# Kernel optimization log

Measured on AMD Instinct MI355X. Metric: run time of the kernel, lower is better.

Reference implementation:

```python
import jax, jax.numpy as jnp
import numpy as np
from functools import partial

MAX_INSTANCES = 8


def _conv(x, W, b):
    y = jax.lax.conv_general_dilated(x, W, (1, 1), 'SAME',
                                     dimension_numbers=('NHWC', 'HWIO', 'NHWC'))
    return jax.nn.relu(y + b)


def _conv_stack(x, params):
    for W, b in params:
        x = _conv(x, W, b)
    return x


def _resize_and_pad(feat, info, bg_h, bg_w):
    # feat: (h, w, c); info: [y1, y2, x1, x2] fractions of bg size.
    # Bilinear resize (half-pixel centers, like tf.image.resize) of feat to
    # (y_size, x_size), then zero-pad into the (bg_h, bg_w) canvas at
    # (y_front, x_front). Expressed as a fixed-shape gather + validity mask
    # so it is jit-compatible despite data-dependent box sizes.
    h, w, _ = feat.shape
    y_size = jnp.maximum((bg_h * (info[1] - info[0])).astype(jnp.int32), 1)
    x_size = jnp.maximum((bg_w * (info[3] - info[2])).astype(jnp.int32), 1)
    y_front = (bg_h * info[0]).astype(jnp.int32)
    x_front = (bg_w * info[2]).astype(jnp.int32)

    def axis(bg_n, front, size, n_in):
        loc = jnp.arange(bg_n) - front
        valid = (loc >= 0) & (loc < size)
        src = (loc.astype(jnp.float32) + 0.5) * (n_in / size.astype(jnp.float32)) - 0.5
        src = jnp.clip(src, 0.0, n_in - 1.0)
        i0 = jnp.floor(src).astype(jnp.int32)
        i1 = jnp.minimum(i0 + 1, n_in - 1)
        return i0, i1, src - i0.astype(jnp.float32), valid

    y0, y1i, fy, vy = axis(bg_h, y_front, y_size, h)
    x0, x1i, fx, vx = axis(bg_w, x_front, x_size, w)
    g = lambda yi, xi: feat[yi][:, xi]  # (bg_h, bg_w, c)
    fy = fy[:, None, None]
    fx = fx[None, :, None]
    out = (g(y0, x0) * (1 - fy) * (1 - fx) + g(y0, x1i) * (1 - fy) * fx
           + g(y1i, x0) * fy * (1 - fx) + g(y1i, x1i) * fy * fx)
    return out * (vy[:, None] & vx[None, :]).astype(feat.dtype)[:, :, None]


def setup_inputs() -> dict:
    key = jax.random.key(0)
    ks = jax.random.split(key, 16)
    B, H, W, C = 4, 128, 128, 64
    h = w = 64
    hm = wm = 56
    U = 64
    MI = MAX_INSTANCES
    instance_feature = jax.random.normal(ks[0], (B, h, w, C, MI), jnp.float32)
    bg_feature = jax.random.normal(ks[1], (B, H, W, C), jnp.float32)
    # Valid boxes: 0 <= y1 < y2 <= 1, 0 <= x1 < x2 <= 1, layout (B, 4, MI).
    y1 = jax.random.uniform(ks[2], (B, 1, MI), minval=0.0, maxval=0.45)
    hh = jax.random.uniform(ks[3], (B, 1, MI), minval=0.2, maxval=0.5)
    x1 = jax.random.uniform(ks[4], (B, 1, MI), minval=0.0, maxval=0.45)
    ww = jax.random.uniform(ks[5], (B, 1, MI), minval=0.2, maxval=0.5)
    bbox = jnp.concatenate([y1, y1 + hh, x1, x1 + ww], axis=1)
    mrcnn_mask = jax.random.uniform(ks[6], (B, hm, wm, MI), jnp.float32)
    s = 0.05  # small weights keep exp() of relu conv outputs well-scaled
    return {
        'instance_feature': instance_feature,
        'bg_feature': bg_feature,
        'bbox': bbox,
        'mrcnn_mask': mrcnn_mask,
        'iW1': jax.random.normal(ks[7], (3, 3, C, U), jnp.float32) * s,
        'ib1': jnp.zeros((U,), jnp.float32),
        'iW2': jax.random.normal(ks[8], (3, 3, U, U), jnp.float32) * s,
        'ib2': jnp.zeros((U,), jnp.float32),
        'iW3': jax.random.normal(ks[9], (3, 3, U, 1), jnp.float32) * s,
        'ib3': jnp.zeros((1,), jnp.float32),
        'bW1': jax.random.normal(ks[10], (3, 3, C, U), jnp.float32) * s,
        'bb1': jnp.zeros((U,), jnp.float32),
        'bW2': jax.random.normal(ks[11], (3, 3, U, U), jnp.float32) * s,
        'bb2': jnp.zeros((U,), jnp.float32),
        'bW3': jax.random.normal(ks[12], (3, 3, U, 1), jnp.float32) * s,
        'bb3': jnp.zeros((1,), jnp.float32),
    }


def reference(instance_feature, bg_feature, bbox, mrcnn_mask,
              iW1, ib1, iW2, ib2, iW3, ib3,
              bW1, bb1, bW2, bb2, bW3, bb3):
    B, H, W, C = bg_feature.shape
    MI = instance_feature.shape[-1]
    h, w = instance_feature.shape[1], instance_feature.shape[2]
    # pack_instance -> conv stack -> unpack (kept as (B, MI, h, w, 1))
    packed = jnp.transpose(instance_feature, (0, 4, 1, 2, 3)).reshape(B * MI, h, w, C)
    iw = _conv_stack(packed, [(iW1, ib1), (iW2, ib2), (iW3, ib3)]).reshape(B, MI, h, w, 1)
    bgw = _conv_stack(bg_feature, [(bW1, bb1), (bW2, bb2), (bW3, bb3)])  # (B,H,W,1)

    rp = jax.vmap(jax.vmap(partial(_resize_and_pad, bg_h=H, bg_w=W)))
    bbox_t = jnp.transpose(bbox, (0, 2, 1))  # (B, MI, 4)
    rw = rp(iw, bbox_t)  # (B, MI, H, W, 1)
    full = jnp.broadcast_to(jnp.array([0.0, 1.0, 0.0, 1.0], jnp.float32), (B, MI, 4))
    rm = rp(jnp.moveaxis(mrcnn_mask, -1, 1)[..., None], full)  # (B, MI, H, W, 1)
    rsf = rp(jnp.moveaxis(instance_feature, -1, 1), bbox_t)  # (B, MI, H, W, C)

    ew = jnp.exp(rw) * rm          # per-instance exp weight, masked
    ew_bg = jnp.exp(bgw)           # (B, H, W, 1)
    denom = ew.sum(axis=1) + ew_bg  # (B, H, W, 1)
    return (ew_bg / denom) * bg_feature + jnp.sum(rsf * (ew / denom[:, None]), axis=1)
```

## Files before the change

### kernel.cpp

```cpp
#include <hip/hip_runtime.h>
#include <cstdint>

typedef short bf16x8 __attribute__((ext_vector_type(8)));
typedef float f32x4 __attribute__((ext_vector_type(4)));
typedef unsigned short u16;
typedef unsigned short u16x8 __attribute__((ext_vector_type(8)));
typedef unsigned int u32;

__device__ inline u16 f2bf(float f) {
  union { float f; unsigned u; } x; x.f = f;
  unsigned u = x.u + 0x7fffu + ((x.u >> 16) & 1u);
  return (u16)(u >> 16);
}
__device__ inline float bf2f(u16 h) {
  union { unsigned u; float f; } x; x.u = ((unsigned)h) << 16;
  return x.f;
}

__global__ __launch_bounds__(256) void prep_kernel(
    const float* __restrict__ inst, u16* __restrict__ pf,
    const float* __restrict__ w0, const float* __restrict__ w1,
    const float* __restrict__ w2, const float* __restrict__ w3,
    u16* __restrict__ wtr,
    const float* __restrict__ bgf, u16* __restrict__ bgp, int nT)
{
  if ((int)blockIdx.x < nT) {
    const int lane = threadIdx.x & 63;
    const int wvid = blockIdx.x * 4 + (threadIdx.x >> 6);
    const int b = wvid >> 12;
    const int pix = wvid & 4095;
    const float* s = inst + ((size_t)(b * 4096 + pix)) * 512 + lane * 8;
    float4 v0 = *(const float4*)s;
    float4 v1 = *(const float4*)(s + 4);
    float vals[8] = {v0.x, v0.y, v0.z, v0.w, v1.x, v1.y, v1.z, v1.w};
    #pragma unroll
    for (int i = 0; i < 8; i++)
      pf[(((size_t)(b * 8 + i)) * 4096 + pix) * 64 + lane] = f2bf(vals[i]);
  } else if ((int)blockIdx.x < nT + 576) {
    int id = (blockIdx.x - nT) * 256 + threadIdx.x;
    if (id >= 147456) return;
    int s = id / 36864;
    int r = id - s * 36864;
    int tap = r >> 12;
    int rc = r & 4095;
    int c = rc >> 6, u = rc & 63;
    const float* Ws = (s == 0) ? w0 : (s == 1) ? w1 : (s == 2) ? w2 : w3;
    wtr[(size_t)s * 36864 + ((size_t)tap * 64 + u) * 64 + c] =
        f2bf(Ws[((size_t)tap * 64 + c) * 64 + u]);
  } else {
    size_t id = (size_t)(blockIdx.x - nT - 576) * 256 + threadIdx.x;
    const float* s = bgf + id * 8;
    float4 v0 = *(const float4*)s;
    float4 v1 = *(const float4*)(s + 4);
    u16x8 o;
    o[0] = f2bf(v0.x); o[1] = f2bf(v0.y); o[2] = f2bf(v0.z); o[3] = f2bf(v0.w);
    o[4] = f2bf(v1.x); o[5] = f2bf(v1.y); o[6] = f2bf(v1.z); o[7] = f2bf(v1.w);
    *(u16x8*)(bgp + id * 8) = o;
  }
}

#define BOFF 41472
template<int SRC>
__device__ __forceinline__ void conv_body(
    char* smem, const void* __restrict__ inv, const u16* __restrict__ wtr,
    const float* __restrict__ bias, u16* __restrict__ out,
    int H, int W, int bid)
{
  const int tilesX = W >> 4;
  const int tilesPerImg = (H >> 4) * tilesX;
  const int img = bid / tilesPerImg;
  const int tile = bid - img * tilesPerImg;
  const int ty = (tile / tilesX) << 4;
  const int tx = (tile % tilesX) << 4;
  const int tid = threadIdx.x;

  for (int idx = tid; idx < 2592; idx += 256) {
    int hpix = idx >> 3;
    int c0 = (idx & 7) << 3;
    int hy = hpix / 18, hx = hpix - hy * 18;
    int gy = ty + hy - 1, gx = tx + hx - 1;
    u16x8 v = {0, 0, 0, 0, 0, 0, 0, 0};
    if (gy >= 0 && gy < H && gx >= 0 && gx < W) {
      if (SRC == 0) {
        const float* s = (const float*)inv + ((size_t)img * H * W + (size_t)gy * W + gx) * 64 + c0;
        #pragma unroll
        for (int j = 0; j < 8; j++) v[j] = f2bf(s[j]);
      } else if (SRC == 1) {
        const u16* s = (const u16*)inv + ((size_t)img * H * W + (size_t)gy * W + gx) * 64 + c0;
        v = *(const u16x8*)s;
      } else {
        int bb = img >> 3, ii = img & 7;
        const float* s = (const float*)inv + ((((size_t)bb * 64 + gy) * 64 + gx) * 64 + c0) * 8 + ii;
        #pragma unroll
        for (int j = 0; j < 8; j++) v[j] = f2bf(s[j * 8]);
      }
    }
    int byte = (hpix * 128 + c0 * 2) ^ ((hpix & 7) << 4);
    *(u16x8*)(smem + byte) = v;
  }

  const int lane = tid & 63;
  const int wv = tid >> 6;
  const int lrow = lane & 15;
  const int kg = lane >> 4;

  const int ch0 = tid, ch1 = tid + 256;
  const int bu0 = ch0 >> 3, bc0 = (ch0 & 7) << 3;
  const int bu1 = ch1 >> 3, bc1 = (ch1 & 7) << 3;
  const int bdst0 = BOFF + ((bu0 * 128 + bc0 * 2) ^ ((bu0 & 7) << 4));
  const int bdst1 = BOFF + ((bu1 * 128 + bc1 * 2) ^ ((bu1 & 7) << 4));

  {
    u16x8 n0 = *(const u16x8*)(wtr + (size_t)(0 * 64 + bu0) * 64 + bc0);
    u16x8 n1 = *(const u16x8*)(wtr + (size_t)(0 * 64 + bu1) * 64 + bc1);
    *(u16x8*)(smem + bdst0) = n0;
    *(u16x8*)(smem + bdst1) = n1;
  }
  __syncthreads();

  int pyv[4], pxv[4];
  #pragma unroll
  for (int mf = 0; mf < 4; mf++) {
    int p = wv * 64 + mf * 16 + lrow;
    pyv[mf] = p >> 4; pxv[mf] = p & 15;
  }

  f32x4 acc[4][4];
  #pragma unroll
  for (int a = 0; a < 4; a++)
    #pragma unroll
    for (int b = 0; b < 4; b++) { f32x4 z = {0.f, 0.f, 0.f, 0.f}; acc[a][b] = z; }

  for (int tap = 0; tap < 9; tap++) {
    u16x8 n0, n1;
    if (tap < 8) {
      n0 = *(const u16x8*)(wtr + (size_t)((tap + 1) * 64 + bu0) * 64 + bc0);
      n1 = *(const u16x8*)(wtr + (size_t)((tap + 1) * 64 + bu1) * 64 + bc1);
    }
    const int ky = tap / 3, kx = tap - ky * 3;
    #pragma unroll
    for (int ks = 0; ks < 2; ks++) {
      bf16x8 Bf[4];
      #pragma unroll
      for (int nf = 0; nf < 4; nf++) {
        int u = nf * 16 + lrow;
        int byte = BOFF + ((u * 128 + ks * 64 + kg * 16) ^ ((u & 7) << 4));
        Bf[nf] = *(const bf16x8*)(smem + byte);
      }
      #pragma unroll
      for (int mf = 0; mf < 4; mf++) {
        int hpix = (pyv[mf] + ky) * 18 + pxv[mf] + kx;
        int byte = (hpix * 128 + ks * 64 + kg * 16) ^ ((hpix & 7) << 4);
        bf16x8 Af = *(const bf16x8*)(smem + byte);
        #pragma unroll
        for (int nf = 0; nf < 4; nf++)
          acc[mf][nf] = __builtin_amdgcn_mfma_f32_16x16x32_bf16(Af, Bf[nf], acc[mf][nf], 0, 0, 0);
      }
    }
    __syncthreads();
    if (tap < 8) {
      *(u16x8*)(smem + bdst0) = n0;
      *(u16x8*)(smem + bdst1) = n1;
      __syncthreads();
    }
  }

  float bv[4];
  #pragma unroll
  for (int nf = 0; nf < 4; nf++) bv[nf] = bias[nf * 16 + lrow];

  const size_t obase = (size_t)img * H * W;
  #pragma unroll
  for (int mf = 0; mf < 4; mf++) {
    #pragma unroll
    for (int j = 0; j < 4; j++) {
      int p = wv * 64 + mf * 16 + kg * 4 + j;
      int oy = ty + (p >> 4), ox = tx + (p & 15);
      u16* op = out + (obase + (size_t)oy * W + ox) * 64 + lrow;
      #pragma unroll
      for (int nf = 0; nf < 4; nf++)
        op[nf * 16] = f2bf(fmaxf(acc[mf][nf][j] + bv[nf], 0.0f));
    }
  }
}

template<int S1, int S2>
__global__ __launch_bounds__(256) void conv_dual(
    const void* in1, const u16* w1, const float* b1, u16* o1, int H1, int W1, int split,
    const void* in2, const u16* w2, const float* b2, u16* o2, int H2, int W2)
{
  extern __shared__ float4 smem_f4[];
  char* smem = (char*)smem_f4;
  if ((int)blockIdx.x < split)
    conv_body<S1>(smem, in1, w1, b1, o1, H1, W1, blockIdx.x);
  else
    conv_body<S2>(smem, in2, w2, b2, o2, H2, W2, blockIdx.x - split);
}

__device__ __forceinline__ void conv3_body(
    char* smem, const u16* __restrict__ in, const float* __restrict__ W3,
    const float* __restrict__ b3, float* __restrict__ out, int H, int W, int bid)
{
  float* wlds = (float*)(smem + 41472);
  const int tilesX = W >> 4;
  const int tilesPerImg = (H >> 4) * tilesX;
  const int img = bid / tilesPerImg;
  const int tile = bid - img * tilesPerImg;
  const int ty = (tile / tilesX) << 4;
  const int tx = (tile % tilesX) << 4;
  const int tid = threadIdx.x;

  for (int idx = tid; idx < 2592; idx += 256) {
    int hpix = idx >> 3;
    int c0 = (idx & 7) << 3;
    int hy = hpix / 18, hx = hpix - hy * 18;
    int gy = ty + hy - 1, gx = tx + hx - 1;
    u16x8 v = {0, 0, 0, 0, 0, 0, 0, 0};
    if (gy >= 0 && gy < H && gx >= 0 && gx < W)
      v = *(const u16x8*)(in + ((size_t)img * H * W + (size_t)gy * W + gx) * 64 + c0);
    int byte = (hpix * 128 + c0 * 2) ^ ((hpix & 7) << 4);
    *(u16x8*)(smem + byte) = v;
  }
  for (int idx = tid; idx < 576; idx += 256) wlds[idx] = W3[idx];
  __syncthreads();

  const int py = tid >> 4, px = tid & 15;
  float acc = 0.0f;
  #pragma unroll
  for (int ky = 0; ky < 3; ky++) {
    #pragma unroll
    for (int kx = 0; kx < 3; kx++) {
      const int hpix = (py + ky) * 18 + (px + kx);
      const float* wp = wlds + (ky * 3 + kx) * 64;
      #pragma unroll
      for (int cg = 0; cg < 8; cg++) {
        int byte = (hpix * 128 + cg * 16) ^ ((hpix & 7) << 4);
        u16x8 v = *(const u16x8*)(smem + byte);
        #pragma unroll
        for (int j = 0; j < 8; j++)
          acc = fmaf(bf2f(v[j]), wp[cg * 8 + j], acc);
      }
    }
  }
  out[(size_t)img * H * W + (size_t)(ty + py) * W + (tx + px)] =
      fmaxf(acc + b3[0], 0.0f);
}

__global__ __launch_bounds__(256) void conv3_dual(
    const u16* in1, const float* W31, const float* b31, float* o1, int H1, int W1, int split,
    const u16* in2, const float* W32, const float* b32, float* o2, int H2, int W2)
{
  extern __shared__ float4 smem_f4[];
  char* smem = (char*)smem_f4;
  if ((int)blockIdx.x < split)
    conv3_body(smem, in1, W31, b31, o1, H1, W1, blockIdx.x);
  else
    conv3_body(smem, in2, W32, b32, o2, H2, W2, blockIdx.x - split);
}

__global__ __launch_bounds__(256) void precompute_params(
    const float* __restrict__ bbox, const float* __restrict__ mask,
    const float* __restrict__ iw, const float* __restrict__ bgw,
    float* __restrict__ pp_wbg, float* __restrict__ pp_wi,
    u32* __restrict__ pp_yx, float* __restrict__ pp_fy, float* __restrict__ pp_fx)
{
  const int gpix = blockIdx.x * 256 + threadIdx.x;
  const int b = gpix >> 14;
  const int p = gpix & 16383;
  const int Y = p >> 7, X = p & 127;

  float msy = ((float)Y + 0.5f) * 0.4375f - 0.5f;
  msy = fminf(fmaxf(msy, 0.0f), 55.0f);
  int my0 = (int)floorf(msy); int my1 = min(my0 + 1, 55); float fmy = msy - (float)my0;
  float msx = ((float)X + 0.5f) * 0.4375f - 0.5f;
  msx = fminf(fmaxf(msx, 0.0f), 55.0f);
  int mx0 = (int)floorf(msx); int mx1 = min(mx0 + 1, 55); float fmx = msx - (float)mx0;

  const float ewbg = expf(bgw[gpix]);
  float denom = ewbg;
  float wi_l[8];
  u32 yx_l[8];
  float fy_l[8], fx_l[8];

  #pragma unroll
  for (int i = 0; i < 8; i++) {
    float by1 = bbox[(b * 4 + 0) * 8 + i];
    float by2 = bbox[(b * 4 + 1) * 8 + i];
    float bx1 = bbox[(b * 4 + 2) * 8 + i];
    float bx2 = bbox[(b * 4 + 3) * 8 + i];
    int ysz = max((int)(128.0f * (by2 - by1)), 1);
    int xsz = max((int)(128.0f * (bx2 - bx1)), 1);
    int yfr = (int)(128.0f * by1);
    int xfr = (int)(128.0f * bx1);
    int ly = Y - yfr, lx = X - xfr;
    bool valid = (ly >= 0) && (ly < ysz) && (lx >= 0) && (lx < xsz);
    float rwv = 0.0f;
    int y0 = 0, y1i = 0, x0 = 0, x1i = 0;
    float fy = 0.0f, fx = 0.0f;
    if (valid) {
      float sy = ((float)ly + 0.5f) * (64.0f / (float)ysz) - 0.5f;
      sy = fminf(fmaxf(sy, 0.0f), 63.0f);
      y0 = (int)floorf(sy); y1i = min(y0 + 1, 63); fy = sy - (float)y0;
      float sx = ((float)lx + 0.5f) * (64.0f / (float)xsz) - 0.5f;
      sx = fminf(fmaxf(sx, 0.0f), 63.0f);
      x0 = (int)floorf(sx); x1i = min(x0 + 1, 63); fx = sx - (float)x0;
      const float* iwp = iw + ((size_t)(b * 8 + i)) * 4096;
      float v00 = iwp[y0 * 64 + x0],  v01 = iwp[y0 * 64 + x1i];
      float v10 = iwp[y1i * 64 + x0], v11 = iwp[y1i * 64 + x1i];
      rwv = v00 * (1.f - fy) * (1.f - fx) + v01 * (1.f - fy) * fx
          + v10 * fy * (1.f - fx)         + v11 * fy * fx;
    }
    const float* mp = mask + (size_t)b * 56 * 56 * 8 + i;
    float m00 = mp[(my0 * 56 + mx0) * 8], m01 = mp[(my0 * 56 + mx1) * 8];
    float m10 = mp[(my1 * 56 + mx0) * 8], m11 = mp[(my1 * 56 + mx1) * 8];
    float rm = m00 * (1.f - fmy) * (1.f - fmx) + m01 * (1.f - fmy) * fmx
             + m10 * fmy * (1.f - fmx)         + m11 * fmy * fmx;
    float ew = expf(rwv) * rm;
    denom += ew;
    wi_l[i] = valid ? ew : 0.0f;
    yx_l[i] = (u32)y0 | ((u32)x0 << 8) | ((u32)y1i << 16) | ((u32)x1i << 24);
    fy_l[i] = fy; fx_l[i] = fx;
  }

  const float invd = 1.0f / denom;
  pp_wbg[gpix] = ewbg * invd;
  #pragma unroll
  for (int i = 0; i < 8; i++) {
    pp_wi[i * 65536 + gpix] = wi_l[i] * invd;
    pp_yx[i * 65536 + gpix] = yx_l[i];
    pp_fy[i * 65536 + gpix] = fy_l[i];
    pp_fx[i * 65536 + gpix] = fx_l[i];
  }
}

__global__ __launch_bounds__(256) void final_blend(
    const u16* __restrict__ pf, const float* __restrict__ bgf,
    const float* __restrict__ pp_wbg, const float* __restrict__ pp_wi,
    const u32* __restrict__ pp_yx, const float* __restrict__ pp_fy,
    const float* __restrict__ pp_fx, float* __restrict__ out)
{
  const int lane = threadIdx.x & 63;
  const int gpix = blockIdx.x * 4 + (threadIdx.x >> 6);
  const int b = gpix >> 14;

  float accv = pp_wbg[gpix] * bgf[(size_t)gpix * 64 + lane];
  #pragma unroll
  for (int i = 0; i < 8; i++) {
    float wiv = pp_wi[i * 65536 + gpix];
    if (wiv != 0.0f) {
      u32 yx = pp_yx[i * 65536 + gpix];
      float fy = pp_fy[i * 65536 + gpix];
      float fx = pp_fx[i * 65536 + gpix];
      int y0 = yx & 255, x0 = (yx >> 8) & 255;
      int y1i = (yx >> 16) & 255, x1i = (yx >> 24) & 255;
      const u16* fp = pf + (size_t)(b * 8 + i) * 262144;
      float g00 = bf2f(fp[((size_t)(y0 * 64 + x0)) * 64 + lane]);
      float g01 = bf2f(fp[((size_t)(y0 * 64 + x1i)) * 64 + lane]);
      float g10 = bf2f(fp[((size_t)(y1i * 64 + x0)) * 64 + lane]);
      float g11 = bf2f(fp[((size_t)(y1i * 64 + x1i)) * 64 + lane]);
      float s = g00 * (1.f - fy) * (1.f - fx) + g01 * (1.f - fy) * fx
              + g10 * fy * (1.f - fx)         + g11 * fy * fx;
      accv = fmaf(wiv, s, accv);
    }
  }
  out[(size_t)gpix * 64 + lane] = accv;
}

__global__ __launch_bounds__(256) void final_kernel_fb(
    const float* __restrict__ inst, const float* __restrict__ bgf,
    const float* __restrict__ bbox, const float* __restrict__ mask,
    const float* __restrict__ iw, const float* __restrict__ bgw,
    float* __restrict__ out)
{
  const int lane = threadIdx.x & 63;
  const int wvid = blockIdx.x * 4 + (threadIdx.x >> 6);
  const int nw = gridDim.x * 4;
  for (int pix = wvid; pix < 4 * 128 * 128; pix += nw) {
    const int b = pix >> 14;
    const int p = pix & 16383;
    const int Y = p >> 7, X = p & 127;

    float msy = ((float)Y + 0.5f) * 0.4375f - 0.5f;
    msy = fminf(fmaxf(msy, 0.0f), 55.0f);
    int my0 = (int)floorf(msy); int my1 = min(my0 + 1, 55); float fmy = msy - (float)my0;
    float msx = ((float)X + 0.5f) * 0.4375f - 0.5f;
    msx = fminf(fmaxf(msx, 0.0f), 55.0f);
    int mx0 = (int)floorf(msx); int mx1 = min(mx0 + 1, 55); float fmx = msx - (float)mx0;

    const float ewbg = expf(bgw[(size_t)b * 16384 + p]);
    float denom = ewbg;
    float acc = 0.0f;

    for (int i = 0; i < 8; i++) {
      float by1 = bbox[(b * 4 + 0) * 8 + i];
      float by2 = bbox[(b * 4 + 1) * 8 + i];
      float bx1 = bbox[(b * 4 + 2) * 8 + i];
      float bx2 = bbox[(b * 4 + 3) * 8 + i];
      int ysz = max((int)(128.0f * (by2 - by1)), 1);
      int xsz = max((int)(128.0f * (bx2 - bx1)), 1);
      int yfr = (int)(128.0f * by1);
      int xfr = (int)(128.0f * bx1);
      int ly = Y - yfr, lx = X - xfr;
      bool valid = (ly >= 0) && (ly < ysz) && (lx >= 0) && (lx < xsz);
      float rwv = 0.0f;
      int y0 = 0, y1i = 0, x0 = 0, x1i = 0;
      float fy = 0.0f, fx = 0.0f;
      if (valid) {
        float sy = ((float)ly + 0.5f) * (64.0f / (float)ysz) - 0.5f;
        sy = fminf(fmaxf(sy, 0.0f), 63.0f);
        y0 = (int)floorf(sy); y1i = min(y0 + 1, 63); fy = sy - (float)y0;
        float sx = ((float)lx + 0.5f) * (64.0f / (float)xsz) - 0.5f;
        sx = fminf(fmaxf(sx, 0.0f), 63.0f);
        x0 = (int)floorf(sx); x1i = min(x0 + 1, 63); fx = sx - (float)x0;
        const float* iwp = iw + ((size_t)(b * 8 + i)) * 4096;
        float v00 = iwp[y0 * 64 + x0],  v01 = iwp[y0 * 64 + x1i];
        float v10 = iwp[y1i * 64 + x0], v11 = iwp[y1i * 64 + x1i];
        rwv = v00 * (1.f - fy) * (1.f - fx) + v01 * (1.f - fy) * fx
            + v10 * fy * (1.f - fx)         + v11 * fy * fx;
      }
      const float* mp = mask + (size_t)b * 56 * 56 * 8 + i;
      float m00 = mp[(my0 * 56 + mx0) * 8], m01 = mp[(my0 * 56 + mx1) * 8];
      float m10 = mp[(my1 * 56 + mx0) * 8], m11 = mp[(my1 * 56 + mx1) * 8];
      float rm = m00 * (1.f - fmy) * (1.f - fmx) + m01 * (1.f - fmy) * fmx
               + m10 * fmy * (1.f - fmx)         + m11 * fmy * fmx;
      float ew = expf(rwv) * rm;
      denom += ew;
      if (valid) {
        const float* fp = inst + (size_t)b * 2097152 + i;
        float g00 = fp[(((size_t)y0 * 64 + x0) * 64 + lane) * 8];
        float g01 = fp[(((size_t)y0 * 64 + x1i) * 64 + lane) * 8];
        float g10 = fp[(((size_t)y1i * 64 + x0) * 64 + lane) * 8];
        float g11 = fp[(((size_t)y1i * 64 + x1i) * 64 + lane) * 8];
        float s = g00 * (1.f - fy) * (1.f - fx) + g01 * (1.f - fy) * fx
                + g10 * fy * (1.f - fx)         + g11 * fy * fx;
        acc += ew * s;
      }
    }
    const float bgv = bgf[((size_t)b * 16384 + p) * 64 + lane];
    out[((size_t)b * 16384 + p) * 64 + lane] = (ewbg * bgv + acc) / denom;
  }
}

extern "C" void kernel_launch(void* const* d_in, const int* in_sizes, int n_in,
                              void* d_out, int out_size, void* d_ws, size_t ws_size,
                              hipStream_t stream) {
  const float* inst = (const float*)d_in[0];
  const float* bgf  = (const float*)d_in[1];
  const float* bbox = (const float*)d_in[2];
  const float* mask = (const float*)d_in[3];
  const float* iW1 = (const float*)d_in[4];  const float* ib1 = (const float*)d_in[5];
  const float* iW2 = (const float*)d_in[6];  const float* ib2 = (const float*)d_in[7];
  const float* iW3 = (const float*)d_in[8];  const float* ib3 = (const float*)d_in[9];
  const float* bW1 = (const float*)d_in[10]; const float* bb1 = (const float*)d_in[11];
  const float* bW2 = (const float*)d_in[12]; const float* bb2 = (const float*)d_in[13];
  const float* bW3 = (const float*)d_in[14]; const float* bb3 = (const float*)d_in[15];

  char* ws = (char*)d_ws;
  u16*   wtr  = (u16*)ws;
  u16*   AbI  = (u16*)(ws + 294912);
  u16*   AbB  = (u16*)(ws + 17072128);
  u16*   BbI  = (u16*)(ws + 25460736);
  u16*   BbB  = (u16*)(ws + 42237952);
  float* iw   = (float*)(ws + 50626560);
  float* bgw  = (float*)(ws + 51150848);
  u16*   pf   = (u16*)(ws + 51412992);
  const bool usePf = ws_size >= (size_t)68190208;
  float* outp = (float*)d_out;

  u16* bgp = BbB;

  float* pp_wbg = (float*)(ws + 294912);
  float* pp_wi  = (float*)(ws + 294912 + 262144);
  u32*   pp_yx  = (u32*)  (ws + 294912 + 2359296);
  float* pp_fy  = (float*)(ws + 294912 + 4456448);
  float* pp_fx  = (float*)(ws + 294912 + 6553600);

  if (usePf) {
    prep_kernel<<<6720, 256, 0, stream>>>(inst, pf, iW1, iW2, bW1, bW2, wtr,
                                          bgf, bgp, 4096);
    conv_dual<1, 1><<<768, 256, 49664, stream>>>(
        pf,  wtr,             ib1, AbI, 64, 64, 512,
        bgp, wtr + 2 * 36864, bb1, AbB, 128, 128);
    conv_dual<1, 1><<<768, 256, 49664, stream>>>(
        AbI, wtr + 36864,     ib2, BbI, 64, 64, 512,
        AbB, wtr + 3 * 36864, bb2, BbB, 128, 128);
    conv3_dual<<<768, 256, 43776, stream>>>(
        BbI, iW3, ib3, iw, 64, 64, 512,
        BbB, bW3, bb3, bgw, 128, 128);
    precompute_params<<<256, 256, 0, stream>>>(bbox, mask, iw, bgw,
        pp_wbg, pp_wi, pp_yx, pp_fy, pp_fx);
    final_blend<<<16384, 256, 0, stream>>>(pf, bgf,
        pp_wbg, pp_wi, pp_yx, pp_fy, pp_fx, outp);
  } else {
    prep_kernel<<<576, 256, 0, stream>>>(inst, pf, iW1, iW2, bW1, bW2, wtr,
                                         bgf, bgp, 0);
    conv_dual<2, 0><<<768, 256, 49664, stream>>>(
        inst, wtr,            ib1, AbI, 64, 64, 512,
        bgf, wtr + 2 * 36864, bb1, AbB, 128, 128);
    conv_dual<1, 1><<<768, 256, 49664, stream>>>(
        AbI, wtr + 36864,     ib2, BbI, 64, 64, 512,
        AbB, wtr + 3 * 36864, bb2, BbB, 128, 128);
    conv3_dual<<<768, 256, 43776, stream>>>(
        BbI, iW3, ib3, iw, 64, 64, 512,
        BbB, bW3, bb3, bgw, 128, 128);
    final_kernel_fb<<<2048, 256, 0, stream>>>(inst, bgf, bbox, mask, iw, bgw, outp);
  }
}
```

Before: 128.3 us.

## Pack blend params into float4 AoS, batch 8 pixels per wave, read bf16 background

precompute_params now writes each pixel's per-instance weight, fractions and packed indices as one float4 in an interleaved layout, instead of four separate strided arrays. final_blend handles 8 pixels per wave and loads each instance's parameters with single vector reads. It reads the background feature from the bf16 copy made in prep, which is now kept in its own workspace region instead of aliasing a conv buffer, rather than from fp32. This cuts parameter and background read traffic in the memory-bound blend stage, but rounds the directly blended background term to bf16 and raises the required workspace size.

```diff
diff --git a/kernel.cpp b/kernel.cpp
--- a/kernel.cpp
+++ b/kernel.cpp
@@ -261,8 +261,7 @@
 __global__ __launch_bounds__(256) void precompute_params(
     const float* __restrict__ bbox, const float* __restrict__ mask,
     const float* __restrict__ iw, const float* __restrict__ bgw,
-    float* __restrict__ pp_wbg, float* __restrict__ pp_wi,
-    u32* __restrict__ pp_yx, float* __restrict__ pp_fy, float* __restrict__ pp_fx)
+    float* __restrict__ pp_wbg, float4* __restrict__ pp_s)
 {
   const int gpix = blockIdx.x * 256 + threadIdx.x;
   const int b = gpix >> 14;
@@ -324,46 +323,58 @@
 
   const float invd = 1.0f / denom;
   pp_wbg[gpix] = ewbg * invd;
+  float4* qs = pp_s + ((size_t)gpix << 3);
   #pragma unroll
   for (int i = 0; i < 8; i++) {
-    pp_wi[i * 65536 + gpix] = wi_l[i] * invd;
-    pp_yx[i * 65536 + gpix] = yx_l[i];
-    pp_fy[i * 65536 + gpix] = fy_l[i];
-    pp_fx[i * 65536 + gpix] = fx_l[i];
+    float4 q;
+    q.x = wi_l[i] * invd;
+    q.y = fy_l[i];
+    q.z = fx_l[i];
+    q.w = __uint_as_float(yx_l[i]);
+    qs[i] = q;
   }
 }
 
 __global__ __launch_bounds__(256) void final_blend(
-    const u16* __restrict__ pf, const float* __restrict__ bgf,
-    const float* __restrict__ pp_wbg, const float* __restrict__ pp_wi,
-    const u32* __restrict__ pp_yx, const float* __restrict__ pp_fy,
-    const float* __restrict__ pp_fx, float* __restrict__ out)
+    const u16* __restrict__ pf, const u16* __restrict__ bgp,
+    const float* __restrict__ pp_wbg, const float4* __restrict__ pp_s,
+    float* __restrict__ out)
 {
   const int lane = threadIdx.x & 63;
-  const int gpix = blockIdx.x * 4 + (threadIdx.x >> 6);
-  const int b = gpix >> 14;
-
-  float accv = pp_wbg[gpix] * bgf[(size_t)gpix * 64 + lane];
-  #pragma unroll
-  for (int i = 0; i < 8; i++) {
-    float wiv = pp_wi[i * 65536 + gpix];
-    if (wiv != 0.0f) {
-      u32 yx = pp_yx[i * 65536 + gpix];
-      float fy = pp_fy[i * 65536 + gpix];
-      float fx = pp_fx[i * 65536 + gpix];
-      int y0 = yx & 255, x0 = (yx >> 8) & 255;
-      int y1i = (yx >> 16) & 255, x1i = (yx >> 24) & 255;
-      const u16* fp = pf + (size_t)(b * 8 + i) * 262144;
-      float g00 = bf2f(fp[((size_t)(y0 * 64 + x0)) * 64 + lane]);
-      float g01 = bf2f(fp[((size_t)(y0 * 64 + x1i)) * 64 + lane]);
-      float g10 = bf2f(fp[((size_t)(y1i * 64 + x0)) * 64 + lane]);
-      float g11 = bf2f(fp[((size_t)(y1i * 64 + x1i)) * 64 + lane]);
-      float s = g00 * (1.f - fy) * (1.f - fx) + g01 * (1.f - fy) * fx
-              + g10 * fy * (1.f - fx)         + g11 * fy * fx;
-      accv = fmaf(wiv, s, accv);
-    }
-  }
-  out[(size_t)gpix * 64 + lane] = accv;
+  const int wave = blockIdx.x * 4 + (threadIdx.x >> 6);
+  const int g0 = wave * 8;
+  const int b = g0 >> 14;
+  const u16* pfb = pf + (size_t)b * 8 * 262144;
+
+  float acc[8];
+  #pragma unroll
+  for (int k = 0; k < 8; k++)
+    acc[k] = pp_wbg[g0 + k] * bf2f(bgp[(size_t)(g0 + k) * 64 + lane]);
+
+  #pragma unroll 2
+  for (int k = 0; k < 8; k++) {
+    const float4* qs = pp_s + ((size_t)(g0 + k) << 3);
+    #pragma unroll
+    for (int i = 0; i < 8; i++) {
+      float4 q = qs[i];
+      if (q.x != 0.0f) {
+        u32 yx = __float_as_uint(q.w);
+        int y0 = yx & 255, x0 = (yx >> 8) & 255;
+        int y1i = (yx >> 16) & 255, x1i = (yx >> 24) & 255;
+        const u16* fp = pfb + (size_t)i * 262144;
+        float g00 = bf2f(fp[((size_t)(y0 * 64 + x0)) * 64 + lane]);
+        float g01 = bf2f(fp[((size_t)(y0 * 64 + x1i)) * 64 + lane]);
+        float g10 = bf2f(fp[((size_t)(y1i * 64 + x0)) * 64 + lane]);
+        float g11 = bf2f(fp[((size_t)(y1i * 64 + x1i)) * 64 + lane]);
+        float s = g00 * (1.f - q.y) * (1.f - q.z) + g01 * (1.f - q.y) * q.z
+                + g10 * q.y * (1.f - q.z)         + g11 * q.y * q.z;
+        acc[k] = fmaf(q.x, s, acc[k]);
+      }
+    }
+  }
+  #pragma unroll
+  for (int k = 0; k < 8; k++)
+    out[(size_t)(g0 + k) * 64 + lane] = acc[k];
 }
 
 __global__ __launch_bounds__(256) void final_kernel_fb(
@@ -464,16 +475,12 @@
   float* iw   = (float*)(ws + 50626560);
   float* bgw  = (float*)(ws + 51150848);
   u16*   pf   = (u16*)(ws + 51412992);
-  const bool usePf = ws_size >= (size_t)68190208;
+  u16*   bgp  = (u16*)(ws + 68190208);
+  const bool usePf = ws_size >= (size_t)76578816;
   float* outp = (float*)d_out;
 
-  u16* bgp = BbB;
-
-  float* pp_wbg = (float*)(ws + 294912);
-  float* pp_wi  = (float*)(ws + 294912 + 262144);
-  u32*   pp_yx  = (u32*)  (ws + 294912 + 2359296);
-  float* pp_fy  = (float*)(ws + 294912 + 4456448);
-  float* pp_fx  = (float*)(ws + 294912 + 6553600);
+  float*  pp_wbg = (float*) (ws + 294912);
+  float4* pp_s   = (float4*)(ws + 294912 + 262144);
 
   if (usePf) {
     prep_kernel<<<6720, 256, 0, stream>>>(inst, pf, iW1, iW2, bW1, bW2, wtr,
@@ -487,10 +494,8 @@
     conv3_dual<<<768, 256, 43776, stream>>>(
         BbI, iW3, ib3, iw, 64, 64, 512,
         BbB, bW3, bb3, bgw, 128, 128);
-    precompute_params<<<256, 256, 0, stream>>>(bbox, mask, iw, bgw,
-        pp_wbg, pp_wi, pp_yx, pp_fy, pp_fx);
-    final_blend<<<16384, 256, 0, stream>>>(pf, bgf,
-        pp_wbg, pp_wi, pp_yx, pp_fy, pp_fx, outp);
+    precompute_params<<<256, 256, 0, stream>>>(bbox, mask, iw, bgw, pp_wbg, pp_s);
+    final_blend<<<2048, 256, 0, stream>>>(pf, bgp, pp_wbg, pp_s, outp);
   } else {
     prep_kernel<<<576, 256, 0, stream>>>(inst, pf, iW1, iW2, bW1, bW2, wtr,
                                          bgf, bgp, 0);
```

After: 137.4 us. 7.1% more time.
